# Kernel tuning notes

Measured on AMD Instinct MI355X. Metric: run time of the kernel, lower is better.

## Reference

```python
import jax, jax.numpy as jnp
import numpy as np

N_EXPERTS = 64
TOP_K = 8
NORM_TOPK = True
SCALING = 1.0


def setup_inputs() -> dict:
    key = jax.random.key(0)
    logits = jax.random.normal(key, (524288, N_EXPERTS), dtype=jnp.float32)
    return {"logits": logits}


def reference(logits):
    # scoring_func == 'softmax': softmax over expert dim in float32
    routing_weights = jax.nn.softmax(logits.astype(jnp.float32), axis=1)
    # top-k experts per token: values and indices, sorted descending (matches torch.topk)
    topk_weights, topk_ids = jax.lax.top_k(routing_weights, TOP_K)  # [T, K]
    if NORM_TOPK:
        topk_weights = topk_weights / jnp.sum(topk_weights, axis=-1, keepdims=True)
    if SCALING != 1.0:
        topk_weights = topk_weights * SCALING
    # torch.histc(topk_ids, bins=E, min=0, max=E) == bincount over flat ids (float output)
    tokens_per_expert = jnp.zeros((N_EXPERTS,), dtype=jnp.float32).at[topk_ids.ravel()].add(1.0)
    return (logits, routing_weights, topk_weights, topk_ids, tokens_per_expert)
```

## Files before the change

### kernel.cpp

```cpp
#include <hip/hip_runtime.h>
#include <math.h>

#define NEXP 64
#define TOPK 8
#define TILE 128
#define PITCH 65
#define MAXGRID 1024

typedef float v4 __attribute__((ext_vector_type(4)));

__global__ __launch_bounds__(TILE) void router_kernel(
    const float* __restrict__ logits,
    float* __restrict__ out_logits,
    float* __restrict__ out_rw,
    float* __restrict__ out_tw,
    float* __restrict__ out_ti,
    float* __restrict__ out_hist,
    int nTiles)
{
    __shared__ float tile[TILE * PITCH];
    __shared__ float SrowInv[TILE];
    __shared__ float shist[NEXP];

    const int tid = threadIdx.x;
    if (tid < NEXP) shist[tid] = 0.0f;

    const int stride = gridDim.x;
    int tb = blockIdx.x;

    v4 pre[16];
    {
        const v4* g = (const v4*)logits + (long)tb * TILE * (NEXP / 4);
        #pragma unroll
        for (int k = 0; k < 16; ++k)
            pre[k] = __builtin_nontemporal_load(&g[tid + TILE * k]);
    }

    for (; tb < nTiles; tb += stride) {
        const long tokBase = (long)tb * TILE;

        v4* gpass = (v4*)out_logits + tokBase * (NEXP / 4);
        #pragma unroll
        for (int k = 0; k < 16; ++k) {
            int i = tid + TILE * k;
            v4 v = pre[k];
            __builtin_nontemporal_store(v, &gpass[i]);
            int r  = i >> 4;
            int c4 = (i & 15) << 2;
            float* b = &tile[r * PITCH + c4];
            b[0] = v.x; b[1] = v.y; b[2] = v.z; b[3] = v.w;
        }
        __syncthreads();

        int nb = tb + stride;
        if (nb < nTiles) {
            const v4* g = (const v4*)logits + (long)nb * TILE * (NEXP / 4);
            #pragma unroll
            for (int k = 0; k < 16; ++k)
                pre[k] = __builtin_nontemporal_load(&g[tid + TILE * k]);
        }

        const float* __restrict__ row = &tile[tid * PITCH];
        float vals[TOPK], ids[TOPK];
        #pragma unroll
        for (int j = 0; j < TOPK; ++j) { vals[j] = -INFINITY; ids[j] = 0.0f; }
        float ssum = 0.0f;

        #pragma unroll 8
        for (int e = 0; e < NEXP; ++e) {
            float x  = row[e];
            ssum += __expf(x);
            float fe = (float)e;
            bool c[TOPK];
            #pragma unroll
            for (int j = 0; j < TOPK; ++j) c[j] = x > vals[j];
            #pragma unroll
            for (int j = TOPK - 1; j >= 1; --j) {
                vals[j] = c[j] ? (c[j - 1] ? vals[j - 1] : x)  : vals[j];
                ids[j]  = c[j] ? (c[j - 1] ? ids[j - 1]  : fe) : ids[j];
            }
            vals[0] = c[0] ? x  : vals[0];
            ids[0]  = c[0] ? fe : ids[0];
        }
        SrowInv[tid] = 1.0f / ssum;

        float ew[TOPK];
        float tsum = 0.0f;
        #pragma unroll
        for (int j = 0; j < TOPK; ++j) { ew[j] = __expf(vals[j]); tsum += ew[j]; }
        const float tinv = 1.0f / tsum;

        const long tok = tokBase + tid;
        v4* twp = (v4*)out_tw + tok * 2;
        v4* tip = (v4*)out_ti + tok * 2;
        v4 w0 = { ew[0]*tinv, ew[1]*tinv, ew[2]*tinv, ew[3]*tinv };
        v4 w1 = { ew[4]*tinv, ew[5]*tinv, ew[6]*tinv, ew[7]*tinv };
        v4 i0 = { ids[0], ids[1], ids[2], ids[3] };
        v4 i1 = { ids[4], ids[5], ids[6], ids[7] };
        __builtin_nontemporal_store(w0, &twp[0]);
        __builtin_nontemporal_store(w1, &twp[1]);
        __builtin_nontemporal_store(i0, &tip[0]);
        __builtin_nontemporal_store(i1, &tip[1]);

        #pragma unroll
        for (int j = 0; j < TOPK; ++j)
            atomicAdd(&shist[(int)ids[j]], 1.0f);

        __syncthreads();

        v4* grw = (v4*)out_rw + tokBase * (NEXP / 4);
        #pragma unroll
        for (int k = 0; k < 16; ++k) {
            int i  = tid + TILE * k;
            int rr = i >> 4;
            int c4 = (i & 15) << 2;
            float si = SrowInv[rr];
            const float* b = &tile[rr * PITCH + c4];
            v4 w;
            w.x = __expf(b[0]) * si;
            w.y = __expf(b[1]) * si;
            w.z = __expf(b[2]) * si;
            w.w = __expf(b[3]) * si;
            __builtin_nontemporal_store(w, &grw[i]);
        }
        __syncthreads();
    }

    if (tid < NEXP) atomicAdd(&out_hist[tid], shist[tid]);
}

extern "C" void kernel_launch(void* const* d_in, const int* in_sizes, int n_in,
                              void* d_out, int out_size, void* d_ws, size_t ws_size,
                              hipStream_t stream) {
    const float* logits = (const float*)d_in[0];
    const long T = (long)in_sizes[0] / NEXP;

    float* out      = (float*)d_out;
    float* o_logits = out;
    float* o_rw     = out + T * NEXP;
    float* o_tw     = out + 2 * T * NEXP;
    float* o_ti     = o_tw + T * TOPK;
    float* o_hist   = o_ti + T * TOPK;

    (void)hipMemsetAsync(o_hist, 0, NEXP * sizeof(float), stream);

    const int nTiles = (int)(T / TILE);
    const int grid   = nTiles < MAXGRID ? nTiles : MAXGRID;
    router_kernel<<<grid, TILE, 0, stream>>>(logits, o_logits, o_rw, o_tw, o_ti,
                                             o_hist, nTiles);
}
```

Measured before the change: 104.1 us.

## Replace LDS-tiled persistent kernel with one-token-per-thread register kernel

Drops the shared-memory tile, the persistent grid-stride loop and the software prefetch. Each thread now loads its token's 64 logits straight into registers, caches the exp values so the softmax output needs no second exp, and uses fmed3 for the top-k insertion. The grid becomes one block of 256 per 256 tokens, which gives 2048 blocks each doing its own shared-histogram flush to global atomics. Per-thread 256-byte contiguous row accesses are not coalesced across the wavefront, and plain stores replace the nontemporal ones, so memory efficiency may drop while LDS traffic and barriers go away.

```diff
diff --git a/kernel.cpp b/kernel.cpp
--- a/kernel.cpp
+++ b/kernel.cpp
@@ -3,129 +3,88 @@
 
 #define NEXP 64
 #define TOPK 8
-#define TILE 128
-#define PITCH 65
-#define MAXGRID 1024
+#define BLK 256
 
 typedef float v4 __attribute__((ext_vector_type(4)));
 
-__global__ __launch_bounds__(TILE) void router_kernel(
+__global__ __launch_bounds__(BLK, 4) void router_kernel(
     const float* __restrict__ logits,
     float* __restrict__ out_logits,
     float* __restrict__ out_rw,
     float* __restrict__ out_tw,
     float* __restrict__ out_ti,
-    float* __restrict__ out_hist,
-    int nTiles)
+    float* __restrict__ out_hist)
 {
-    __shared__ float tile[TILE * PITCH];
-    __shared__ float SrowInv[TILE];
     __shared__ float shist[NEXP];
-
     const int tid = threadIdx.x;
     if (tid < NEXP) shist[tid] = 0.0f;
+    __syncthreads();
 
-    const int stride = gridDim.x;
-    int tb = blockIdx.x;
+    const long tok = (long)blockIdx.x * BLK + tid;
 
-    v4 pre[16];
-    {
-        const v4* g = (const v4*)logits + (long)tb * TILE * (NEXP / 4);
+    const v4* g = (const v4*)logits + tok * (NEXP / 4);
+    v4 row[16];
+    #pragma unroll
+    for (int k = 0; k < 16; ++k) row[k] = g[k];
+
+    v4* gp = (v4*)out_logits + tok * (NEXP / 4);
+    #pragma unroll
+    for (int k = 0; k < 16; ++k) gp[k] = row[k];
+
+    float vals[TOPK], ids[TOPK];
+    #pragma unroll
+    for (int j = 0; j < TOPK; ++j) { vals[j] = -INFINITY; ids[j] = 0.0f; }
+    float ssum = 0.0f;
+
+    #pragma unroll
+    for (int e = 0; e < NEXP; ++e) {
+        float x  = row[e >> 2][e & 3];
+        float ev = __expf(x);
+        ssum += ev;
+        row[e >> 2][e & 3] = ev;
+        float fe = (float)e;
+        bool c[TOPK];
         #pragma unroll
-        for (int k = 0; k < 16; ++k)
-            pre[k] = __builtin_nontemporal_load(&g[tid + TILE * k]);
+        for (int j = 0; j < TOPK; ++j) c[j] = x > vals[j];
+        #pragma unroll
+        for (int j = TOPK - 1; j >= 1; --j) {
+            ids[j]  = c[j] ? (c[j - 1] ? ids[j - 1] : fe) : ids[j];
+            vals[j] = __builtin_amdgcn_fmed3f(x, vals[j - 1], vals[j]);
+        }
+        ids[0]  = c[0] ? fe : ids[0];
+        vals[0] = fmaxf(vals[0], x);
+    }
+    const float sinv = 1.0f / ssum;
+
+    float ew[TOPK];
+    float tsum = 0.0f;
+    #pragma unroll
+    for (int j = 0; j < TOPK; ++j) { ew[j] = __expf(vals[j]); tsum += ew[j]; }
+    const float tinv = 1.0f / tsum;
+
+    v4* twp = (v4*)out_tw + tok * 2;
+    v4* tip = (v4*)out_ti + tok * 2;
+    v4 w0 = { ew[0] * tinv, ew[1] * tinv, ew[2] * tinv, ew[3] * tinv };
+    v4 w1 = { ew[4] * tinv, ew[5] * tinv, ew[6] * tinv, ew[7] * tinv };
+    v4 i0 = { ids[0], ids[1], ids[2], ids[3] };
+    v4 i1 = { ids[4], ids[5], ids[6], ids[7] };
+    __builtin_nontemporal_store(w0, &twp[0]);
+    __builtin_nontemporal_store(w1, &twp[1]);
+    __builtin_nontemporal_store(i0, &tip[0]);
+    __builtin_nontemporal_store(i1, &tip[1]);
+
+    v4* grw = (v4*)out_rw + tok * (NEXP / 4);
+    #pragma unroll
+    for (int k = 0; k < 16; ++k) {
+        v4 w = row[k];
+        w.x *= sinv; w.y *= sinv; w.z *= sinv; w.w *= sinv;
+        grw[k] = w;
     }
 
-    for (; tb < nTiles; tb += stride) {
-        const long tokBase = (long)tb * TILE;
-
-        v4* gpass = (v4*)out_logits + tokBase * (NEXP / 4);
-        #pragma unroll
-        for (int k = 0; k < 16; ++k) {
-            int i = tid + TILE * k;
-            v4 v = pre[k];
-            __builtin_nontemporal_store(v, &gpass[i]);
-            int r  = i >> 4;
-            int c4 = (i & 15) << 2;
-            float* b = &tile[r * PITCH + c4];
-            b[0] = v.x; b[1] = v.y; b[2] = v.z; b[3] = v.w;
-        }
-        __syncthreads();
-
-        int nb = tb + stride;
-        if (nb < nTiles) {
-            const v4* g = (const v4*)logits + (long)nb * TILE * (NEXP / 4);
-            #pragma unroll
-            for (int k = 0; k < 16; ++k)
-                pre[k] = __builtin_nontemporal_load(&g[tid + TILE * k]);
-        }
-
-        const float* __restrict__ row = &tile[tid * PITCH];
-        float vals[TOPK], ids[TOPK];
-        #pragma unroll
-        for (int j = 0; j < TOPK; ++j) { vals[j] = -INFINITY; ids[j] = 0.0f; }
-        float ssum = 0.0f;
-
-        #pragma unroll 8
-        for (int e = 0; e < NEXP; ++e) {
-            float x  = row[e];
-            ssum += __expf(x);
-            float fe = (float)e;
-            bool c[TOPK];
-            #pragma unroll
-            for (int j = 0; j < TOPK; ++j) c[j] = x > vals[j];
-            #pragma unroll
-            for (int j = TOPK - 1; j >= 1; --j) {
-                vals[j] = c[j] ? (c[j - 1] ? vals[j - 1] : x)  : vals[j];
-                ids[j]  = c[j] ? (c[j - 1] ? ids[j - 1]  : fe) : ids[j];
-            }
-            vals[0] = c[0] ? x  : vals[0];
-            ids[0]  = c[0] ? fe : ids[0];
-        }
-        SrowInv[tid] = 1.0f / ssum;
-
-        float ew[TOPK];
-        float tsum = 0.0f;
-        #pragma unroll
-        for (int j = 0; j < TOPK; ++j) { ew[j] = __expf(vals[j]); tsum += ew[j]; }
-        const float tinv = 1.0f / tsum;
-
-        const long tok = tokBase + tid;
-        v4* twp = (v4*)out_tw + tok * 2;
-        v4* tip = (v4*)out_ti + tok * 2;
-        v4 w0 = { ew[0]*tinv, ew[1]*tinv, ew[2]*tinv, ew[3]*tinv };
-        v4 w1 = { ew[4]*tinv, ew[5]*tinv, ew[6]*tinv, ew[7]*tinv };
-        v4 i0 = { ids[0], ids[1], ids[2], ids[3] };
-        v4 i1 = { ids[4], ids[5], ids[6], ids[7] };
-        __builtin_nontemporal_store(w0, &twp[0]);
-        __builtin_nontemporal_store(w1, &twp[1]);
-        __builtin_nontemporal_store(i0, &tip[0]);
-        __builtin_nontemporal_store(i1, &tip[1]);
-
-        #pragma unroll
-        for (int j = 0; j < TOPK; ++j)
-            atomicAdd(&shist[(int)ids[j]], 1.0f);
-
-        __syncthreads();
-
-        v4* grw = (v4*)out_rw + tokBase * (NEXP / 4);
-        #pragma unroll
-        for (int k = 0; k < 16; ++k) {
-            int i  = tid + TILE * k;
-            int rr = i >> 4;
-            int c4 = (i & 15) << 2;
-            float si = SrowInv[rr];
-            const float* b = &tile[rr * PITCH + c4];
-            v4 w;
-            w.x = __expf(b[0]) * si;
-            w.y = __expf(b[1]) * si;
-            w.z = __expf(b[2]) * si;
-            w.w = __expf(b[3]) * si;
-            __builtin_nontemporal_store(w, &grw[i]);
-        }
-        __syncthreads();
-    }
-
+    #pragma unroll
+    for (int j = 0; j < TOPK; ++j)
+        atomicAdd(&shist[(int)ids[j]], 1.0f);
+    __syncthreads();
     if (tid < NEXP) atomicAdd(&out_hist[tid], shist[tid]);
 }
 
@@ -144,8 +103,7 @@
 
     (void)hipMemsetAsync(o_hist, 0, NEXP * sizeof(float), stream);
 
-    const int nTiles = (int)(T / TILE);
-    const int grid   = nTiles < MAXGRID ? nTiles : MAXGRID;
-    router_kernel<<<grid, TILE, 0, stream>>>(logits, o_logits, o_rw, o_tw, o_ti,
-                                             o_hist, nTiles);
+    const int grid = (int)(T / BLK);
+    router_kernel<<<grid, BLK, 0, stream>>>(logits, o_logits, o_rw, o_tw, o_ti,
+                                            o_hist);
 }
```

After: 162.3 us. +55.9%, slower.
